# Optimization experiments

Hardware: AMD Instinct MI355X
Metric: run time of the kernel (lower is better)

## Reference

```python
import jax, jax.numpy as jnp
import numpy as np

B, T, M, S, D, H, DH, P = 4, 1024, 1024, 1024, 1024, 16, 64, 4096


def layernorm(x, g, b, eps=1e-5):
    mu = x.mean(-1, keepdims=True)
    var = ((x - mu) ** 2).mean(-1, keepdims=True)
    return (x - mu) * jax.lax.rsqrt(var + eps) * g + b


def rel_shift(x):
    # Transformer-XL relative shift on [B,H,q,k] BD scores
    b, h, q, k = x.shape
    x = jnp.pad(x, ((0, 0), (0, 0), (0, 0), (1, 0)))
    return x.reshape(b, h, k + 1, q)[:, :, 1:, :].reshape(b, h, q, k)


def rel_attention(x, kv, mem, mask, pos_emb, r_w_bias, r_r_bias,
                  Wq, Wk, Wv, Wr, Wo, g, bln):
    # x: [B,Tq,D] queries; kv: [B,Skv,D]; mem: optional [B,M,D]
    cat = kv if mem is None else jnp.concatenate([mem, kv], axis=1)
    Bb, Tq, _ = x.shape
    K = cat.shape[1]
    q = (x @ Wq).reshape(Bb, Tq, H, DH)
    k = (cat @ Wk).reshape(Bb, K, H, DH)
    v = (cat @ Wv).reshape(Bb, K, H, DH)
    r = (pos_emb[-K:] @ Wr).reshape(K, H, DH)  # rel-pos keys, most-recent K positions
    AC = jnp.einsum('bthd,bkhd->bhtk', q + r_w_bias, k)
    BD = rel_shift(jnp.einsum('bthd,khd->bhtk', q + r_r_bias, r))
    scores = (AC + BD) * (1.0 / np.sqrt(DH))
    scores = jnp.where(mask[:, None, :, :], jnp.asarray(-1e30, scores.dtype), scores)
    prob = jax.nn.softmax(scores, axis=-1)
    o = jnp.einsum('bhtk,bkhd->bthd', prob, v).reshape(Bb, Tq, H * DH) @ Wo
    return layernorm(x + o, g, bln), cat, prob  # post-LN residual; cat is new memory


def residual_ff(x, W1, b1, W2, b2, g, bln):
    h = jax.nn.relu(x @ W1 + b1) @ W2 + b2
    return layernorm(x + h, g, bln)


def setup_inputs() -> dict:
    key = jax.random.key(0)
    ks = jax.random.split(key, 24)
    w = lambda i, shape: jax.random.normal(ks[i], shape, jnp.float32) * 0.02
    causal = jnp.triu(jnp.ones((T, M + T), bool), k=M + 1)  # True = masked
    return {
        'src': jax.random.normal(ks[0], (B, S, D), jnp.float32),
        'tgt': jax.random.normal(ks[1], (B, T, D), jnp.float32),
        'tgt_mem': jax.random.normal(ks[2], (B, M, D), jnp.float32),
        'pos_emb': w(3, (M + T, D)),
        'r_w_bias': w(4, (H, DH)),
        'r_r_bias': w(5, (H, DH)),
        'Wq1': w(6, (D, H * DH)), 'Wk1': w(7, (D, H * DH)), 'Wv1': w(8, (D, H * DH)),
        'Wr1': w(9, (D, H * DH)), 'Wo1': w(10, (H * DH, D)),
        'ln1_g': jnp.ones((D,), jnp.float32), 'ln1_b': jnp.zeros((D,), jnp.float32),
        'Wq2': w(11, (D, H * DH)), 'Wk2': w(12, (D, H * DH)), 'Wv2': w(13, (D, H * DH)),
        'Wr2': w(14, (D, H * DH)), 'Wo2': w(15, (H * DH, D)),
        'ln2_g': jnp.ones((D,), jnp.float32), 'ln2_b': jnp.zeros((D,), jnp.float32),
        'Wf1': w(16, (D, P)), 'bf1': jnp.zeros((P,), jnp.float32),
        'Wf2': w(17, (P, D)), 'bf2': jnp.zeros((D,), jnp.float32),
        'ln3_g': jnp.ones((D,), jnp.float32), 'ln3_b': jnp.zeros((D,), jnp.float32),
        'tgt_mask': jnp.broadcast_to(causal, (B, T, M + T)),
        'tgt_to_src_mask': jnp.zeros((B, T, S), bool),
    }


def reference(src, tgt, tgt_mem, pos_emb, r_w_bias, r_r_bias,
              Wq1, Wk1, Wv1, Wr1, Wo1, ln1_g, ln1_b,
              Wq2, Wk2, Wv2, Wr2, Wo2, ln2_g, ln2_b,
              Wf1, bf1, Wf2, bf2, ln3_g, ln3_b,
              tgt_mask, tgt_to_src_mask):
    out, new_mem, self_att_prob = rel_attention(
        tgt, tgt, tgt_mem, tgt_mask, pos_emb, r_w_bias, r_r_bias,
        Wq1, Wk1, Wv1, Wr1, Wo1, ln1_g, ln1_b)
    out, _, inter_att_prob = rel_attention(
        out, src, None, tgt_to_src_mask, pos_emb, r_w_bias, r_r_bias,
        Wq2, Wk2, Wv2, Wr2, Wo2, ln2_g, ln2_b)
    out = residual_ff(out, Wf1, bf1, Wf2, bf2, ln3_g, ln3_b)
    return (out, new_mem, self_att_prob, inter_att_prob)
```

## Files before the change

kernel.cpp:

```cpp
#include <hip/hip_runtime.h>

typedef unsigned short u16;
typedef __attribute__((ext_vector_type(8))) short short8;
typedef __attribute__((ext_vector_type(4))) float f4;
typedef __attribute__((ext_vector_type(4))) unsigned short u16x4;

__device__ __forceinline__ float b2f(u16 u) {
    unsigned int x = ((unsigned int)u) << 16;
    return __builtin_bit_cast(float, x);
}
__device__ __forceinline__ u16 f2b(float f) {
    unsigned int u = __builtin_bit_cast(unsigned int, f);
    u += 0x7FFFu + ((u >> 16) & 1u);
    return (u16)(u >> 16);
}

__device__ __forceinline__ void gl16(const void* g, void* l) {
    __builtin_amdgcn_global_load_lds(
        (const __attribute__((address_space(1))) void*)g,
        (__attribute__((address_space(3))) void*)l, 16, 0, 0);
}

template<int FM, int FN, int CBF, int EPI>
__global__ __launch_bounds__(256, 3)
void gemm_bt(const u16* __restrict__ Ap, const u16* __restrict__ Bp,
             void* __restrict__ Cp, const float* __restrict__ bias,
             int M, int N, int K, int lda, int ldb, int ldc,
             long long sAh, long long sAb, long long sBh, long long sBb,
             long long sCh, long long sCb, int batchH)
{
    constexpr int BM = FM * 32;
    constexpr int BN = FN * 32;
    __shared__ __align__(16) u16 As[2][BM * 32];
    __shared__ __align__(16) u16 Bs[2][BN * 32];

    const int tid  = threadIdx.x;
    const int z    = blockIdx.z;
    const int bb   = z / batchH;
    const int hh   = z - bb * batchH;
    const int m0   = blockIdx.y * BM;
    const int n0   = blockIdx.x * BN;
    const int w    = tid >> 6;
    const int lane = tid & 63;
    const int wr   = w >> 1;
    const int wc   = w & 1;
    const int lrow = lane & 15;
    const int lk   = (lane >> 4) << 3;
    const int lrow4 = lane >> 2;
    const int lch   = lane & 3;

    const u16* Ag = Ap + sAb * bb + sAh * hh;
    const u16* Bg = Bp + sBb * bb + sBh * hh;

    f4 acc[FM][FN] = {};

    auto stage = [&](int buf, int kt) {
        const int kb = kt << 5;
        #pragma unroll
        for (int i = 0; i < BM / 64; ++i) {
            const int row0 = (w + i * 4) << 4;
            gl16(Ag + (long long)(m0 + row0 + lrow4) * lda + kb + (lch << 3),
                 &As[buf][row0 * 32]);
        }
        #pragma unroll
        for (int i = 0; i < BN / 64; ++i) {
            const int row0 = (w + i * 4) << 4;
            gl16(Bg + (long long)(n0 + row0 + lrow4) * ldb + kb + (lch << 3),
                 &Bs[buf][row0 * 32]);
        }
    };

    const int nKt = K >> 5;
    stage(0, 0);
    __syncthreads();
    int cur = 0;
    for (int kt = 0; kt < nKt; ++kt) {
        if (kt + 1 < nKt) stage(cur ^ 1, kt + 1);

        short8 af[FM], bv[FN];
        #pragma unroll
        for (int m = 0; m < FM; ++m)
            af[m] = *(const short8*)(&As[cur][(wr * FM * 16 + m * 16 + lrow) * 32 + lk]);
        #pragma unroll
        for (int n = 0; n < FN; ++n)
            bv[n] = *(const short8*)(&Bs[cur][(wc * FN * 16 + n * 16 + lrow) * 32 + lk]);
        #pragma unroll
        for (int m = 0; m < FM; ++m)
            #pragma unroll
            for (int n = 0; n < FN; ++n)
                acc[m][n] = __builtin_amdgcn_mfma_f32_16x16x32_bf16(af[m], bv[n], acc[m][n], 0, 0, 0);

        __syncthreads();
        cur ^= 1;
    }

    const int crow0 = m0 + wr * FM * 16 + ((lane >> 4) << 2);
    const int ccol0 = n0 + wc * FN * 16 + lrow;
    if (CBF == 0) {
        float* Cg = (float*)Cp + sCb * bb + sCh * hh;
        #pragma unroll
        for (int m = 0; m < FM; ++m) {
            #pragma unroll
            for (int n = 0; n < FN; ++n) {
                const int col = ccol0 + n * 16;
                float bvv = (EPI >= 1) ? bias[col] : 0.f;
                #pragma unroll
                for (int r = 0; r < 4; ++r) {
                    float vv = acc[m][n][r] + bvv;
                    if (EPI == 2) vv = fmaxf(vv, 0.f);
                    Cg[(long long)(crow0 + m * 16 + r) * ldc + col] = vv;
                }
            }
        }
    } else {
        u16* Cg = (u16*)Cp + sCb * bb + sCh * hh;
        #pragma unroll
        for (int m = 0; m < FM; ++m) {
            #pragma unroll
            for (int n = 0; n < FN; ++n) {
                const int col = ccol0 + n * 16;
                float bvv = (EPI >= 1) ? bias[col] : 0.f;
                #pragma unroll
                for (int r = 0; r < 4; ++r) {
                    float vv = acc[m][n][r] + bvv;
                    if (EPI == 2) vv = fmaxf(vv, 0.f);
                    Cg[(long long)(crow0 + m * 16 + r) * ldc + col] = f2b(vv);
                }
            }
        }
    }
}

template<int KK, int MODE>
__global__ __launch_bounds__(512, 4)
void fattn(const u16* __restrict__ qsrc, long long qld, long long qsb,
           const float* __restrict__ rwb, const float* __restrict__ rrb,
           const u16* __restrict__ kb, const u16* __restrict__ rr,
           const u16* __restrict__ vt,
           float* __restrict__ probs, u16* __restrict__ ob, int kld)
{
    constexpr int LE = KK + 8;
    constexpr int NT = KK / 16;
    constexpr int NI = NT / 8;
    constexpr int NB = NI / 4;
    __shared__ __align__(16) u16 e[16 * LE];
    __shared__ __align__(16) u16 qws[16 * 72];
    __shared__ __align__(16) u16 qrs[17 * 72];
    __shared__ float psum[8][16];

    const int tid = threadIdx.x;
    const int bid = blockIdx.x;
    const int nid = ((bid & 7) << 9) + (bid >> 3);
    const int bh  = nid >> 6;
    const int t0  = (nid & 63) << 4;
    const int b   = bh >> 4, h = bh & 15;

    if (tid < 264) {
        int row, ch; const float* bias; u16* dst; bool act = true;
        if (tid < 128)      { row = tid >> 3;        ch = tid & 7; bias = rwb; dst = &qws[row * 72 + ch * 8]; }
        else if (tid < 256) { row = (tid - 128) >> 3; ch = tid & 7; bias = rrb; dst = &qrs[row * 72 + ch * 8]; }
        else if (MODE == 1) { row = 16;              ch = tid - 256; bias = rrb; dst = &qrs[16 * 72 + ch * 8]; }
        else act = false;
        if (act) {
            int trow = t0 + row; if (trow > 1023) trow = 1023;
            short8 qv = *(const short8*)(qsrc + b * qsb + (long long)trow * qld + h * 64 + ch * 8);
            const float* bp = bias + h * 64 + ch * 8;
            f4 b0 = *(const f4*)bp, b1 = *(const f4*)(bp + 4);
            short8 o;
            o[0] = (short)f2b((b2f((u16)qv[0]) + b0.x) * 0.125f);
            o[1] = (short)f2b((b2f((u16)qv[1]) + b0.y) * 0.125f);
            o[2] = (short)f2b((b2f((u16)qv[2]) + b0.z) * 0.125f);
            o[3] = (short)f2b((b2f((u16)qv[3]) + b0.w) * 0.125f);
            o[4] = (short)f2b((b2f((u16)qv[4]) + b1.x) * 0.125f);
            o[5] = (short)f2b((b2f((u16)qv[5]) + b1.y) * 0.125f);
            o[6] = (short)f2b((b2f((u16)qv[6]) + b1.z) * 0.125f);
            o[7] = (short)f2b((b2f((u16)qv[7]) + b1.w) * 0.125f);
            *(short8*)dst = o;
        }
    }
    __syncthreads();

    const int w = tid >> 6, lane = tid & 63;
    const int lc = lane & 15, g = lane >> 4, lk = g << 3;
    const int t = t0 + lc;

    const short8 bq0 = *(const short8*)&qws[lc * 72 + lk];
    const short8 bq1 = *(const short8*)&qws[lc * 72 + 32 + lk];
    const short8 br0 = *(const short8*)&qrs[lc * 72 + lk];
    const short8 br1 = *(const short8*)&qrs[lc * 72 + 32 + lk];
    short8 bs0 = {}, bs1 = {};
    if (MODE == 1) {
        bs0 = *(const short8*)&qrs[(lc + 1) * 72 + lk];
        bs1 = *(const short8*)&qrs[(lc + 1) * 72 + 32 + lk];
    }

    #pragma unroll
    for (int Bb = 0; Bb < NI; Bb += 2) {
        short8 R0[2], R1[2];
        #pragma unroll
        for (int u = 0; u < 2; ++u) {
            const int ut = w + (Bb + u) * 8;
            const int u0 = ut << 4;
            const bool nd = (u0 + t0 + 30 >= 1023) || (MODE == 1 && u0 + t0 <= 1021);
            if (nd) {
                const u16* rg = rr + (long long)(u0 + lc) * 2048 + h * 64;
                R0[u] = *(const short8*)(rg + lk);
                R1[u] = *(const short8*)(rg + 32 + lk);
            }
        }
        #pragma unroll
        for (int u = 0; u < 2; ++u) {
            const int ut = w + (Bb + u) * 8;
            const int u0 = ut << 4;
            const bool need1 = (u0 + t0 + 30 >= 1023);
            const bool need2 = (MODE == 1) && (u0 + t0 <= 1021);
            if (need1) {
                f4 acc = {};
                acc = __builtin_amdgcn_mfma_f32_16x16x32_bf16(R0[u], br0, acc, 0, 0, 0);
                acc = __builtin_amdgcn_mfma_f32_16x16x32_bf16(R1[u], br1, acc, 0, 0, 0);
                #pragma unroll
                for (int i = 0; i < 4; ++i) {
                    const int j = u0 + 4 * g + i + t - 1023;
                    if (j >= 0) e[lc * LE + j] = f2b(acc[i]);
                }
            }
            if (MODE == 1 && need2) {
                f4 acc = {};
                acc = __builtin_amdgcn_mfma_f32_16x16x32_bf16(R0[u], bs0, acc, 0, 0, 0);
                acc = __builtin_amdgcn_mfma_f32_16x16x32_bf16(R1[u], bs1, acc, 0, 0, 0);
                #pragma unroll
                for (int i = 0; i < 4; ++i) {
                    const int j = u0 + 4 * g + i + t + 2;
                    if (j < KK) e[lc * LE + j] = f2b(acc[i]);
                }
            }
        }
    }
    __syncthreads();

    float sum = 0.f;
    const int limit = t + 1024;
    const int jvt = (MODE == 0) ? ((t0 + 1039) >> 4) : (NT - 1);
    {
        short8 K0a[4], K0b[4], K1c[4];
        auto ldK0 = [&](short8* dst, int B2) {
            #pragma unroll
            for (int u = 0; u < 4; ++u) {
                const int jt = w + (B2 * 4 + u) * 8;
                if (MODE != 0 || jt <= jvt) {
                    const u16* kg = kb + (long long)(b * KK + (jt << 4) + lc) * kld + h * 64;
                    dst[u] = *(const short8*)(kg + lk);
                }
            }
        };
        ldK0(K0a, 0);
        #pragma unroll
        for (int B2 = 0; B2 < NB; ++B2) {
            short8* K0c = (B2 & 1) ? K0b : K0a;
            short8* K0n = (B2 & 1) ? K0a : K0b;
            #pragma unroll
            for (int u = 0; u < 4; ++u) {
                const int jt = w + (B2 * 4 + u) * 8;
                if (MODE != 0 || jt <= jvt) {
                    const u16* kg = kb + (long long)(b * KK + (jt << 4) + lc) * kld + h * 64;
                    K1c[u] = *(const short8*)(kg + 32 + lk);
                }
            }
            if (B2 + 1 < NB) ldK0(K0n, B2 + 1);
            __builtin_amdgcn_s_setprio(1);
            #pragma unroll
            for (int u = 0; u < 4; ++u) {
                const int jt = w + (B2 * 4 + u) * 8;
                const int jme = (jt << 4) + 4 * g;
                if (MODE == 0 && jt > jvt) {
                    u16x4 z = {0, 0, 0, 0};
                    *(u16x4*)&e[lc * LE + jme] = z;
                } else {
                    f4 acc = {};
                    acc = __builtin_amdgcn_mfma_f32_16x16x32_bf16(K0c[u], bq0, acc, 0, 0, 0);
                    acc = __builtin_amdgcn_mfma_f32_16x16x32_bf16(K1c[u], bq1, acc, 0, 0, 0);
                    u16x4 bd4 = *(const u16x4*)&e[lc * LE + jme];
                    u16x4 st;
                    #pragma unroll
                    for (int i = 0; i < 4; ++i) {
                        const int j = jme + i;
                        float bd = b2f(bd4[i]);
                        if (MODE == 1 && j == t + 1) bd = 0.f;
                        float ev = __expf(acc[i] + bd);
                        if (MODE == 0 && j > limit) ev = 0.f;
                        sum += ev;
                        st[i] = f2b(ev);
                    }
                    *(u16x4*)&e[lc * LE + jme] = st;
                }
            }
            __builtin_amdgcn_s_setprio(0);
        }
    }
    sum += __shfl_xor(sum, 16);
    sum += __shfl_xor(sum, 32);
    if (g == 0) psum[w][lc] = sum;
    __syncthreads();

    if (w >= 4) {
        const int r = (tid >> 4) & 15;
        const int q = tid & 15;
        float s = 0.f;
        #pragma unroll
        for (int w2 = 0; w2 < 8; ++w2) s += psum[w2][r];
        const float inv = 1.f / s;
        float* pr = probs + ((long long)bh * 1024 + t0 + r) * KK;
        #pragma unroll 4
        for (int i2 = 0; i2 < KK / 128; ++i2) {
            const int j0 = q * 8 + i2 * 128;
            u16x4 e0 = *(const u16x4*)&e[r * LE + j0];
            u16x4 e1 = *(const u16x4*)&e[r * LE + j0 + 4];
            f4 p0, p1;
            p0.x = b2f(e0.x) * inv; p0.y = b2f(e0.y) * inv;
            p0.z = b2f(e0.z) * inv; p0.w = b2f(e0.w) * inv;
            p1.x = b2f(e1.x) * inv; p1.y = b2f(e1.y) * inv;
            p1.z = b2f(e1.z) * inv; p1.w = b2f(e1.w) * inv;
            __builtin_nontemporal_store(p0, (f4*)(pr + j0));
            __builtin_nontemporal_store(p1, (f4*)(pr + j0 + 4));
        }
    } else {
        const int db = w << 4;
        const u16* vrow = vt + ((long long)(bh * 64 + db + lc)) * KK + lk;
        int kcend = KK / 32;
        if (MODE == 0) {
            const int ke = (t0 + 1071) >> 5;
            if (ke < kcend) kcend = ke;
        }
        f4 acc = {};
        __builtin_amdgcn_s_setprio(1);
        #pragma unroll 2
        for (int kc = 0; kc < kcend; ++kc) {
            short8 a = *(const short8*)&e[lc * LE + kc * 32 + lk];
            short8 bv = *(const short8*)(vrow + kc * 32);
            acc = __builtin_amdgcn_mfma_f32_16x16x32_bf16(a, bv, acc, 0, 0, 0);
        }
        __builtin_amdgcn_s_setprio(0);
        #pragma unroll
        for (int i = 0; i < 4; ++i) {
            const int trow = g * 4 + i;
            float s = 0.f;
            #pragma unroll
            for (int w2 = 0; w2 < 8; ++w2) s += psum[w2][trow];
            ob[((long long)(b * 1024 + t0 + trow)) * 1024 + h * 64 + db + lc] = f2b(acc[i] / s);
        }
    }
}

__global__ void prep0(const float* __restrict__ mem, const float* __restrict__ tgt,
                      const float* __restrict__ src, const float* __restrict__ pos,
                      float* __restrict__ nm, u16* __restrict__ cat,
                      u16* __restrict__ srcb, u16* __restrict__ posb)
{
    const int bid = blockIdx.x;
    const int tid = threadIdx.x;
    if (bid < 8192) {
        long long i = (long long)bid * 256 + tid;
        long long b = i >> 19;
        int rem = (int)(i & 524287);
        int r = rem >> 8, c4 = rem & 255;
        const float* sp = (r < 1024) ? (mem + ((b << 10) + r) * 1024 + c4 * 4)
                                     : (tgt + ((b << 10) + (r - 1024)) * 1024 + c4 * 4);
        f4 v = *(const f4*)sp;
        __builtin_nontemporal_store(v, (f4*)(nm + i * 4));
        u16x4 o; o.x = f2b(v.x); o.y = f2b(v.y); o.z = f2b(v.z); o.w = f2b(v.w);
        *(u16x4*)(cat + i * 4) = o;
    } else if (bid < 12288) {
        long long i = (long long)(bid - 8192) * 256 + tid;
        f4 v = *(const f4*)(src + i * 4);
        u16x4 o; o.x = f2b(v.x); o.y = f2b(v.y); o.z = f2b(v.z); o.w = f2b(v.w);
        *(u16x4*)(srcb + i * 4) = o;
    } else {
        long long i = (long long)(bid - 12288) * 256 + tid;
        f4 v = *(const f4*)(pos + i * 4);
        u16x4 o; o.x = f2b(v.x); o.y = f2b(v.y); o.z = f2b(v.z); o.w = f2b(v.w);
        *(u16x4*)(posb + i * 4) = o;
    }
}

struct TWS { const float* s; u16* d; int sld, dld; };
struct TW18 { TWS t[18]; };
__global__ void transpose_w18(TW18 p)
{
    __shared__ float tile[32][33];
    const TWS ts = p.t[blockIdx.z];
    int c0 = blockIdx.x * 32, r0 = blockIdx.y * 32;
    int tx = threadIdx.x, ty = threadIdx.y;
    tile[ty][tx] = ts.s[(long long)(r0 + ty) * ts.sld + c0 + tx];
    __syncthreads();
    ts.d[(long long)(c0 + ty) * ts.dld + r0 + tx] = f2b(tile[tx][ty]);
}

__global__ __launch_bounds__(256) void transpose_v(const u16* __restrict__ v, u16* __restrict__ vt,
                                                   int KK, int ld, int coff)
{
    __shared__ u16 tile[64][68];
    const int z = blockIdx.z, b = z >> 4, h = z & 15;
    const int j0 = blockIdx.x << 6;
    const int rr8 = threadIdx.x >> 3;
    const int c8 = (threadIdx.x & 7) << 3;
    #pragma unroll
    for (int p = 0; p < 2; ++p) {
        const int jr = p * 32 + rr8;
        short8 val = *(const short8*)(v + ((long long)(b * KK + j0 + jr)) * ld + coff + h * 64 + c8);
        #pragma unroll
        for (int k = 0; k < 8; ++k) tile[c8 + k][jr] = (u16)val[k];
    }
    __syncthreads();
    #pragma unroll
    for (int p = 0; p < 2; ++p) {
        const int d = p * 32 + rr8;
        short8 o;
        #pragma unroll
        for (int k = 0; k < 8; ++k) o[k] = (short)tile[d][c8 + k];
        *(short8*)(vt + ((long long)((b * 16 + h) * 64 + d)) * KK + j0 + c8) = o;
    }
}

__global__ __launch_bounds__(256) void ln_res(const float* __restrict__ x,
                                              const float* __restrict__ h1,
                                              const float* __restrict__ h2,
                                              const float* __restrict__ hbias,
                                              const float* __restrict__ g, const float* __restrict__ bl,
                                              float* __restrict__ o32, u16* __restrict__ obf)
{
    const long long row = blockIdx.x;
    const int tid = threadIdx.x;
    const long long base = row * 1024 + tid * 4;
    f4 xa = *(const f4*)(x + base);
    f4 ha = *(const f4*)(h1 + base);
    f4 hb = *(const f4*)(h2 + base);
    f4 hc = {0.f, 0.f, 0.f, 0.f};
    if (hbias) hc = *(const f4*)(hbias + tid * 4);
    float v0 = xa.x + ha.x + hb.x + hc.x, v1 = xa.y + ha.y + hb.y + hc.y;
    float v2 = xa.z + ha.z + hb.z + hc.z, v3 = xa.w + ha.w + hb.w + hc.w;
    float lsum = v0 + v1 + v2 + v3;
    float lsq = v0 * v0 + v1 * v1 + v2 * v2 + v3 * v3;
    #pragma unroll
    for (int o2 = 32; o2; o2 >>= 1) { lsum += __shfl_xor(lsum, o2); lsq += __shfl_xor(lsq, o2); }
    __shared__ float r1[4], r2[4];
    int w = tid >> 6, lane = tid & 63;
    if (lane == 0) { r1[w] = lsum; r2[w] = lsq; }
    __syncthreads();
    lsum = r1[0] + r1[1] + r1[2] + r1[3];
    lsq  = r2[0] + r2[1] + r2[2] + r2[3];
    const float mu = lsum * 0.0009765625f;
    const float var = lsq * 0.0009765625f - mu * mu;
    const float rsd = rsqrtf(var + 1e-5f);
    const int c = tid * 4;
    f4 gv = *(const f4*)(g + c);
    f4 bv = *(const f4*)(bl + c);
    f4 y;
    y.x = (v0 - mu) * rsd * gv.x + bv.x;
    y.y = (v1 - mu) * rsd * gv.y + bv.y;
    y.z = (v2 - mu) * rsd * gv.z + bv.z;
    y.w = (v3 - mu) * rsd * gv.w + bv.w;
    *(f4*)(o32 + base) = y;
    if (obf) {
        u16x4 u; u.x = f2b(y.x); u.y = f2b(y.y); u.z = f2b(y.z); u.w = f2b(y.w);
        *(u16x4*)(obf + base) = u;
    }
}

extern "C" void kernel_launch(void* const* d_in, const int* in_sizes, int n_in,
                              void* d_out, int out_size, void* d_ws, size_t ws_size,
                              hipStream_t stream)
{
    (void)in_sizes; (void)n_in; (void)out_size;
    const float* src  = (const float*)d_in[0];
    const float* tgt  = (const float*)d_in[1];
    const float* mem  = (const float*)d_in[2];
    const float* pos  = (const float*)d_in[3];
    const float* rwb  = (const float*)d_in[4];
    const float* rrb  = (const float*)d_in[5];
    const float* Wq1  = (const float*)d_in[6];
    const float* Wk1  = (const float*)d_in[7];
    const float* Wv1  = (const float*)d_in[8];
    const float* Wr1  = (const float*)d_in[9];
    const float* Wo1  = (const float*)d_in[10];
    const float* ln1g = (const float*)d_in[11];
    const float* ln1b = (const float*)d_in[12];
    const float* Wq2  = (const float*)d_in[13];
    const float* Wk2  = (const float*)d_in[14];
    const float* Wv2  = (const float*)d_in[15];
    const float* Wr2  = (const float*)d_in[16];
    const float* Wo2  = (const float*)d_in[17];
    const float* ln2g = (const float*)d_in[18];
    const float* ln2b = (const float*)d_in[19];
    const float* Wf1  = (const float*)d_in[20];
    const float* bf1  = (const float*)d_in[21];
    const float* Wf2  = (const float*)d_in[22];
    const float* bf2  = (const float*)d_in[23];
    const float* ln3g = (const float*)d_in[24];
    const float* ln3b = (const float*)d_in[25];

    float* outp   = (float*)d_out;
    float* newmem = outp + 4194304;
    float* selfP  = outp + 12582912;
    float* interP = outp + 146800640;

    char* ws = (char*)d_ws;
    size_t off = 0;
    auto alloc = [&](size_t bytes) -> void* {
        void* p = ws + off;
        off = (off + bytes + 255) & ~(size_t)255;
        return p;
    };
    u16*   src_bf  = (u16*)alloc(8u << 20);
    u16*   cat_bf  = (u16*)alloc(16u << 20);
    u16*   pos_bf  = (u16*)alloc(4u << 20);
    u16*   W1t    = (u16*)alloc(6u << 20);
    u16*   Wr12t  = (u16*)alloc(4u << 20);
    u16*   W2t    = (u16*)alloc(4u << 20);
    u16*   Wq2t   = (u16*)alloc(2u << 20);
    u16*   Wo1t   = (u16*)alloc(2u << 20);
    u16*   Wo2t   = (u16*)alloc(2u << 20);
    u16*   Wf1t   = (u16*)alloc(8u << 20);
    u16*   Wf2t   = (u16*)alloc(8u << 20);
    u16*   P1kv   = (u16*)alloc(34u << 20);
    u16*   qb1    = (u16*)alloc(8u << 20);
    u16*   P2k    = (u16*)alloc(8u << 20);
    u16*   P2v    = (u16*)alloc(8u << 20);
    u16*   R12    = (u16*)alloc(8u << 20);
    u16*   qb2    = (u16*)alloc(8u << 20);
    u16*   vtb    = (u16*)alloc(16u << 20);
    u16*   ob     = (u16*)alloc(8u << 20);
    float* projb  = (float*)alloc(16u << 20);
    float* projb2 = (float*)alloc(16u << 20);
    float* out1_32 = (float*)alloc(16u << 20);
    u16*   out1_bf = (u16*)alloc(8u << 20);
    float* out2_32 = (float*)alloc(16u << 20);
    u16*   out2_bf = (u16*)alloc(8u << 20);
    u16*   hb     = (u16*)alloc(32u << 20);
    if (off > ws_size) return;
    const long long PJ2 = projb2 - projb;

    dim3 tb(32, 32);

    prep0<<<14336, 256, 0, stream>>>(mem, tgt, src, pos, newmem, cat_bf, src_bf, pos_bf);
    TW18 tw;
    tw.t[0] = {Wq1, W1t, 1024, 1024};
    tw.t[1] = {Wk1, W1t + 1048576, 1024, 1024};
    tw.t[2] = {Wv1, W1t + 2097152, 1024, 1024};
    tw.t[3] = {Wr1, Wr12t, 1024, 1024};
    tw.t[4] = {Wr2, Wr12t + 1048576, 1024, 1024};
    tw.t[5] = {Wk2, W2t, 1024, 1024};
    tw.t[6] = {Wv2, W2t + 1048576, 1024, 1024};
    tw.t[7] = {Wq2, Wq2t, 1024, 1024};
    tw.t[8] = {Wo1, Wo1t, 1024, 1024};
    tw.t[9] = {Wo2, Wo2t, 1024, 1024};
    for (int zz = 0; zz < 4; ++zz) {
        tw.t[10 + zz] = {Wf1 + zz * 1024, Wf1t + (long long)zz * 1048576, 4096, 1024};
        tw.t[14 + zz] = {Wf2 + (long long)zz * 1048576, Wf2t + zz * 1024, 1024, 4096};
    }
    transpose_w18<<<dim3(32, 32, 18), tb, 0, stream>>>(tw);

    gemm_bt<4,4,1,0><<<dim3(16,64,1), 256, 0, stream>>>(cat_bf, W1t + 1048576, P1kv, nullptr,
        8192,2048,1024, 1024,1024,2080, 0,0,0,0,0,0, 1);
    gemm_bt<2,4,1,0><<<dim3(8,16,4), 256, 0, stream>>>(cat_bf + 1048576, W1t, qb1, nullptr,
        1024,1024,1024, 1024,1024,1024, 0,2048LL*1024, 0,0, 0,1048576LL, 1);
    gemm_bt<2,4,1,0><<<dim3(16,32,1), 256, 0, stream>>>(pos_bf, Wr12t, R12, nullptr,
        2048,2048,1024, 1024,1024,2048, 0,0,0,0,0,0, 1);
    transpose_v<<<dim3(32,1,64), 256, 0, stream>>>(P1kv, vtb, 2048, 2080, 1024);
    fattn<2048,0><<<4096, 512, 0, stream>>>(qb1, 1024LL, 1048576LL,
        rwb, rrb, P1kv, R12, vtb, selfP, ob, 2080);
    gemm_bt<2,4,0,0><<<dim3(8,64,2), 256, 0, stream>>>(ob, Wo1t, projb, nullptr,
        4096,1024,512, 1024,1024,1024, 0,512, 0,512, 0,PJ2, 1);
    ln_res<<<4096, 256, 0, stream>>>(tgt, projb, projb2, nullptr, ln1g, ln1b, out1_32, out1_bf);

    {
        const long long dA = (long long)(src_bf - out1_bf);
        const long long dB1 = (long long)(W2t - Wq2t);
        const long long dB2 = (long long)((W2t + 1048576) - Wq2t);
        const long long dC1 = (long long)(P2k - qb2);
        const long long dC2 = (long long)(P2v - qb2);
        gemm_bt<2,4,1,0><<<dim3(8,64,3), 256, 0, stream>>>(out1_bf, Wq2t, qb2, nullptr,
            4096,1024,1024, 1024,1024,1024, dA,dA, dB1,dB2, dC1,dC2, 2);
    }
    transpose_v<<<dim3(16,1,64), 256, 0, stream>>>(P2v, vtb, 1024, 1024, 0);
    fattn<1024,1><<<4096, 512, 0, stream>>>(qb2, 1024LL, 1048576LL,
        rwb, rrb, P2k, R12 + 1024LL * 2048 + 1024, vtb, interP, ob, 1024);
    gemm_bt<2,4,0,0><<<dim3(8,64,2), 256, 0, stream>>>(ob, Wo2t, projb, nullptr,
        4096,1024,512, 1024,1024,1024, 0,512, 0,512, 0,PJ2, 1);
    ln_res<<<4096, 256, 0, stream>>>(out1_32, projb, projb2, nullptr, ln2g, ln2b, out2_32, out2_bf);

    gemm_bt<4,4,1,2><<<dim3(32,32,1), 256, 0, stream>>>(out2_bf, Wf1t, hb, bf1,
        4096,4096,1024, 1024,1024,4096, 0,0,0,0,0,0, 1);
    gemm_bt<2,4,0,0><<<dim3(8,64,2), 256, 0, stream>>>(hb, Wf2t, projb, nullptr,
        4096,1024,2048, 4096,4096,1024, 0,2048, 0,2048, 0,PJ2, 1);
    ln_res<<<4096, 256, 0, stream>>>(out2_32, projb, projb2, bf2, ln3g, ln3b, outp, nullptr);
}
```

Baseline: 898.2 us.

## Fuse V transpose into GEMM epilogue and drop split-K for output projections

Adds a GEMM epilogue mode that writes the V projection directly in transposed per-head layout, so the separate transpose_v kernels and the staging V buffers go away. The self-attention K and V projections become separate GEMMs, and the K buffer gets a narrower leading dimension. The Wo1, Wo2 and Wf2 projections switch from two-way split-K with two partial fp32 outputs to a single full-K GEMM, so LayerNorm reads one projection buffer. The trade-off is fewer blocks in those GEMMs, which may hurt occupancy, and scattered 8-byte transposed stores in the V epilogue.

```diff
diff --git a/kernel.cpp b/kernel.cpp
--- a/kernel.cpp
+++ b/kernel.cpp
@@ -112,7 +112,7 @@
                 }
             }
         }
-    } else {
+    } else if (CBF == 1) {
         u16* Cg = (u16*)Cp + sCb * bb + sCh * hh;
         #pragma unroll
         for (int m = 0; m < FM; ++m) {
@@ -126,6 +126,22 @@
                     if (EPI == 2) vv = fmaxf(vv, 0.f);
                     Cg[(long long)(crow0 + m * 16 + r) * ldc + col] = f2b(vv);
                 }
+            }
+        }
+    } else {
+        u16* Cg = (u16*)Cp;
+        #pragma unroll
+        for (int m = 0; m < FM; ++m) {
+            const int row0 = crow0 + m * 16;
+            const int b2 = row0 / ldc;
+            const int j = row0 - b2 * ldc;
+            #pragma unroll
+            for (int n = 0; n < FN; ++n) {
+                const int col = ccol0 + n * 16;
+                u16x4 o;
+                o.x = f2b(acc[m][n][0]); o.y = f2b(acc[m][n][1]);
+                o.z = f2b(acc[m][n][2]); o.w = f2b(acc[m][n][3]);
+                *(u16x4*)(Cg + ((long long)(b2 * 1024 + col)) * ldc + j) = o;
             }
         }
     }
@@ -395,32 +411,6 @@
     ts.d[(long long)(c0 + ty) * ts.dld + r0 + tx] = f2b(tile[tx][ty]);
 }
 
-__global__ __launch_bounds__(256) void transpose_v(const u16* __restrict__ v, u16* __restrict__ vt,
-                                                   int KK, int ld, int coff)
-{
-    __shared__ u16 tile[64][68];
-    const int z = blockIdx.z, b = z >> 4, h = z & 15;
-    const int j0 = blockIdx.x << 6;
-    const int rr8 = threadIdx.x >> 3;
-    const int c8 = (threadIdx.x & 7) << 3;
-    #pragma unroll
-    for (int p = 0; p < 2; ++p) {
-        const int jr = p * 32 + rr8;
-        short8 val = *(const short8*)(v + ((long long)(b * KK + j0 + jr)) * ld + coff + h * 64 + c8);
-        #pragma unroll
-        for (int k = 0; k < 8; ++k) tile[c8 + k][jr] = (u16)val[k];
-    }
-    __syncthreads();
-    #pragma unroll
-    for (int p = 0; p < 2; ++p) {
-        const int d = p * 32 + rr8;
-        short8 o;
-        #pragma unroll
-        for (int k = 0; k < 8; ++k) o[k] = (short)tile[d][c8 + k];
-        *(short8*)(vt + ((long long)((b * 16 + h) * 64 + d)) * KK + j0 + c8) = o;
-    }
-}
-
 __global__ __launch_bounds__(256) void ln_res(const float* __restrict__ x,
                                               const float* __restrict__ h1,
                                               const float* __restrict__ h2,
@@ -433,7 +423,8 @@
     const long long base = row * 1024 + tid * 4;
     f4 xa = *(const f4*)(x + base);
     f4 ha = *(const f4*)(h1 + base);
-    f4 hb = *(const f4*)(h2 + base);
+    f4 hb = {0.f, 0.f, 0.f, 0.f};
+    if (h2) hb = *(const f4*)(h2 + base);
     f4 hc = {0.f, 0.f, 0.f, 0.f};
     if (hbias) hc = *(const f4*)(hbias + tid * 4);
     float v0 = xa.x + ha.x + hb.x + hc.x, v1 = xa.y + ha.y + hb.y + hc.y;
@@ -521,23 +512,20 @@
     u16*   Wo2t   = (u16*)alloc(2u << 20);
     u16*   Wf1t   = (u16*)alloc(8u << 20);
     u16*   Wf2t   = (u16*)alloc(8u << 20);
-    u16*   P1kv   = (u16*)alloc(34u << 20);
+    u16*   K1b    = (u16*)alloc(18u << 20);
     u16*   qb1    = (u16*)alloc(8u << 20);
     u16*   P2k    = (u16*)alloc(8u << 20);
-    u16*   P2v    = (u16*)alloc(8u << 20);
     u16*   R12    = (u16*)alloc(8u << 20);
     u16*   qb2    = (u16*)alloc(8u << 20);
     u16*   vtb    = (u16*)alloc(16u << 20);
     u16*   ob     = (u16*)alloc(8u << 20);
     float* projb  = (float*)alloc(16u << 20);
-    float* projb2 = (float*)alloc(16u << 20);
     float* out1_32 = (float*)alloc(16u << 20);
     u16*   out1_bf = (u16*)alloc(8u << 20);
     float* out2_32 = (float*)alloc(16u << 20);
     u16*   out2_bf = (u16*)alloc(8u << 20);
     u16*   hb     = (u16*)alloc(32u << 20);
     if (off > ws_size) return;
-    const long long PJ2 = projb2 - projb;
 
     dim3 tb(32, 32);
 
@@ -559,38 +547,38 @@
     }
     transpose_w18<<<dim3(32, 32, 18), tb, 0, stream>>>(tw);
 
-    gemm_bt<4,4,1,0><<<dim3(16,64,1), 256, 0, stream>>>(cat_bf, W1t + 1048576, P1kv, nullptr,
-        8192,2048,1024, 1024,1024,2080, 0,0,0,0,0,0, 1);
+    gemm_bt<4,4,1,0><<<dim3(8,64,1), 256, 0, stream>>>(cat_bf, W1t + 1048576, K1b, nullptr,
+        8192,1024,1024, 1024,1024,1056, 0,0,0,0,0,0, 1);
+    gemm_bt<4,4,2,0><<<dim3(8,64,1), 256, 0, stream>>>(cat_bf, W1t + 2097152, vtb, nullptr,
+        8192,1024,1024, 1024,1024,2048, 0,0,0,0,0,0, 1);
     gemm_bt<2,4,1,0><<<dim3(8,16,4), 256, 0, stream>>>(cat_bf + 1048576, W1t, qb1, nullptr,
         1024,1024,1024, 1024,1024,1024, 0,2048LL*1024, 0,0, 0,1048576LL, 1);
     gemm_bt<2,4,1,0><<<dim3(16,32,1), 256, 0, stream>>>(pos_bf, Wr12t, R12, nullptr,
         2048,2048,1024, 1024,1024,2048, 0,0,0,0,0,0, 1);
-    transpose_v<<<dim3(32,1,64), 256, 0, stream>>>(P1kv, vtb, 2048, 2080, 1024);
     fattn<2048,0><<<4096, 512, 0, stream>>>(qb1, 1024LL, 1048576LL,
-        rwb, rrb, P1kv, R12, vtb, selfP, ob, 2080);
-    gemm_bt<2,4,0,0><<<dim3(8,64,2), 256, 0, stream>>>(ob, Wo1t, projb, nullptr,
-        4096,1024,512, 1024,1024,1024, 0,512, 0,512, 0,PJ2, 1);
-    ln_res<<<4096, 256, 0, stream>>>(tgt, projb, projb2, nullptr, ln1g, ln1b, out1_32, out1_bf);
+        rwb, rrb, K1b, R12, vtb, selfP, ob, 1056);
+    gemm_bt<2,4,0,0><<<dim3(8,64,1), 256, 0, stream>>>(ob, Wo1t, projb, nullptr,
+        4096,1024,1024, 1024,1024,1024, 0,0,0,0,0,0, 1);
+    ln_res<<<4096, 256, 0, stream>>>(tgt, projb, nullptr, nullptr, ln1g, ln1b, out1_32, out1_bf);
 
     {
         const long long dA = (long long)(src_bf - out1_bf);
-        const long long dB1 = (long long)(W2t - Wq2t);
-        const long long dB2 = (long long)((W2t + 1048576) - Wq2t);
-        const long long dC1 = (long long)(P2k - qb2);
-        const long long dC2 = (long long)(P2v - qb2);
-        gemm_bt<2,4,1,0><<<dim3(8,64,3), 256, 0, stream>>>(out1_bf, Wq2t, qb2, nullptr,
-            4096,1024,1024, 1024,1024,1024, dA,dA, dB1,dB2, dC1,dC2, 2);
-    }
-    transpose_v<<<dim3(16,1,64), 256, 0, stream>>>(P2v, vtb, 1024, 1024, 0);
+        const long long dB = (long long)(W2t - Wq2t);
+        const long long dC = (long long)(P2k - qb2);
+        gemm_bt<2,4,1,0><<<dim3(8,64,2), 256, 0, stream>>>(out1_bf, Wq2t, qb2, nullptr,
+            4096,1024,1024, 1024,1024,1024, 0,dA, 0,dB, 0,dC, 1);
+    }
+    gemm_bt<2,4,2,0><<<dim3(8,64,1), 256, 0, stream>>>(src_bf, W2t + 1048576, vtb, nullptr,
+        4096,1024,1024, 1024,1024,1024, 0,0,0,0,0,0, 1);
     fattn<1024,1><<<4096, 512, 0, stream>>>(qb2, 1024LL, 1048576LL,
         rwb, rrb, P2k, R12 + 1024LL * 2048 + 1024, vtb, interP, ob, 1024);
-    gemm_bt<2,4,0,0><<<dim3(8,64,2), 256, 0, stream>>>(ob, Wo2t, projb, nullptr,
-        4096,1024,512, 1024,1024,1024, 0,512, 0,512, 0,PJ2, 1);
-    ln_res<<<4096, 256, 0, stream>>>(out1_32, projb, projb2, nullptr, ln2g, ln2b, out2_32, out2_bf);
+    gemm_bt<2,4,0,0><<<dim3(8,64,1), 256, 0, stream>>>(ob, Wo2t, projb, nullptr,
+        4096,1024,1024, 1024,1024,1024, 0,0,0,0,0,0, 1);
+    ln_res<<<4096, 256, 0, stream>>>(out1_32, projb, nullptr, nullptr, ln2g, ln2b, out2_32, out2_bf);
 
     gemm_bt<4,4,1,2><<<dim3(32,32,1), 256, 0, stream>>>(out2_bf, Wf1t, hb, bf1,
         4096,4096,1024, 1024,1024,4096, 0,0,0,0,0,0, 1);
-    gemm_bt<2,4,0,0><<<dim3(8,64,2), 256, 0, stream>>>(hb, Wf2t, projb, nullptr,
-        4096,1024,2048, 4096,4096,1024, 0,2048, 0,2048, 0,PJ2, 1);
-    ln_res<<<4096, 256, 0, stream>>>(out2_32, projb, projb2, bf2, ln3g, ln3b, outp, nullptr);
-}
+    gemm_bt<2,4,0,0><<<dim3(8,64,1), 256, 0, stream>>>(hb, Wf2t, projb, nullptr,
+        4096,1024,4096, 4096,4096,1024, 0,0,0,0,0,0, 1);
+    ln_res<<<4096, 256, 0, stream>>>(out2_32, projb, nullptr, bf2, ln3g, ln3b, outp, nullptr);
+}
```

Measured after the change: 891.4 us. About the same (-0.8%).
